# Optimization experiments

Hardware: AMD Instinct MI355X
Metric: run time of the kernel (lower is better)

Reference implementation:

```python
import jax, jax.numpy as jnp
import numpy as np

HEADS = 16
D_MODEL = 1024
D_K = D_MODEL // HEADS


def setup_inputs() -> dict:
    key = jax.random.key(0)
    ks = jax.random.split(key, 8)
    B, S = 4, 2048
    scale = 1.0 / np.sqrt(D_MODEL)
    return {
        "queries": jax.random.normal(ks[0], (B, S, D_MODEL), dtype=jnp.float32),
        "keys": jax.random.normal(ks[1], (B, S, D_MODEL), dtype=jnp.float32),
        "values": jax.random.normal(ks[2], (B, S, D_MODEL), dtype=jnp.float32),
        # Per-head projection weights, stacked over heads: [H, d_model, d_k]
        "Wq": jax.random.normal(ks[3], (HEADS, D_MODEL, D_K), dtype=jnp.float32) * scale,
        "Wk": jax.random.normal(ks[4], (HEADS, D_MODEL, D_K), dtype=jnp.float32) * scale,
        "Wv": jax.random.normal(ks[5], (HEADS, D_MODEL, D_K), dtype=jnp.float32) * scale,
        "Wout": jax.random.normal(ks[6], (D_MODEL, D_MODEL), dtype=jnp.float32) * scale,
        "bout": jax.random.normal(ks[7], (D_MODEL,), dtype=jnp.float32) * 0.01,
    }


def reference(queries, keys, values, Wq, Wk, Wv, Wout, bout):
    # Per-head linear projections (torch Linear: x @ W.T, here W stored as [H, d_model, d_k])
    q = jnp.einsum("bsd,hdk->bhsk", queries, Wq)   # [B,H,S,d_k]
    k = jnp.einsum("btd,hdk->bhtk", keys, Wk)      # [B,H,T,d_k]
    v = jnp.einsum("btd,hdv->bhtv", values, Wv)    # [B,H,T,d_v]
    scores = jnp.einsum("bhsk,bhtk->bhst", q, k) / jnp.sqrt(jnp.float32(D_K))
    probs = jax.nn.softmax(scores, axis=-1)        # [B,H,S,T]
    wv = jnp.einsum("bhst,bhtv->bhsv", probs, v)   # [B,H,S,d_v]
    # concat heads along last dim: [B,S,H*d_v] == [B,S,d_model]
    B, H, S, Dv = wv.shape
    concat = jnp.transpose(wv, (0, 2, 1, 3)).reshape(B, S, H * Dv)
    return concat @ Wout.T + bout
```

## Files before the change

### kernel.cpp

```cpp
#include <hip/hip_runtime.h>
#include <hip/hip_bf16.h>
#include <stdint.h>

#define DM 1024
#define SZ ((size_t)8192*1024)
#define WSZ ((size_t)1024*1024)

typedef float  f32x4  __attribute__((ext_vector_type(4)));
typedef float  f32x16 __attribute__((ext_vector_type(16)));
typedef __bf16 bf16x8 __attribute__((ext_vector_type(8)));
typedef __bf16 bf16x2 __attribute__((ext_vector_type(2)));
typedef short  s16x8  __attribute__((ext_vector_type(8)));
typedef unsigned int u32;
typedef unsigned int u32x4 __attribute__((ext_vector_type(4)));

typedef const __attribute__((address_space(1))) void* gas_ptr;
typedef __attribute__((address_space(3))) void* las_ptr;

static __device__ __forceinline__ f32x4 mfma16(s16x8 a, s16x8 b, f32x4 c){
  return __builtin_amdgcn_mfma_f32_16x16x32_bf16(
      __builtin_bit_cast(bf16x8, a), __builtin_bit_cast(bf16x8, b), c, 0, 0, 0);
}
static __device__ __forceinline__ f32x16 mfma32(s16x8 a, s16x8 b, f32x16 c){
  return __builtin_amdgcn_mfma_f32_32x32x16_bf16(
      __builtin_bit_cast(bf16x8, a), __builtin_bit_cast(bf16x8, b), c, 0, 0, 0);
}

static __device__ __forceinline__ u32 pack2(float a, float b){
  bf16x2 v = { (__bf16)a, (__bf16)b };
  return __builtin_bit_cast(u32, v);
}
static __device__ __forceinline__ short f2bf(float f){
  __bf16 v = (__bf16)f;
  return __builtin_bit_cast(short, v);
}

static __device__ __forceinline__ void gload_lds16(void* l, const void* g){
  __builtin_amdgcn_global_load_lds((gas_ptr)g, (las_ptr)l, 16, 0, 0);
}

#define QSCALE 0.1803368801111444f


__global__ void convert_misc(const float* __restrict__ q, const float* __restrict__ k,
                             const float* __restrict__ v, const float* __restrict__ wo,
                             short* __restrict__ ws){
  size_t c = (size_t)blockIdx.x*blockDim.x + threadIdx.x;
  const size_t n8_in = 3*(SZ/8);
  const float* src; short* dst;
  if (c < n8_in){
    int s = (int)(c >> 20);
    size_t off = c*8 - ((size_t)s << 23);
    src = (s==0 ? q : (s==1 ? k : v)) + off;
    dst = ws + c*8;
  } else {
    size_t off = (c - n8_in)*8;
    src = wo + off;
    dst = ws + 6*SZ + 3*WSZ + off;
  }
  float4 a = *(const float4*)src;
  float4 b = *(const float4*)(src + 4);
  uint4 o;
  o.x = pack2(a.x, a.y); o.y = pack2(a.z, a.w);
  o.z = pack2(b.x, b.y); o.w = pack2(b.z, b.w);
  *(uint4*)dst = o;
}

__global__ void convert_wqkv(const float* __restrict__ wq, const float* __restrict__ wk,
                             const float* __restrict__ wv, short* __restrict__ ws){
  __shared__ float tile[64][65];
  int bid = blockIdx.x;
  int sel = bid >> 8;
  int h   = (bid >> 4) & 15;
  int dt  = bid & 15;
  const float* W = sel==0 ? wq : (sel==1 ? wk : wv);
  float sc = sel==0 ? QSCALE : 1.0f;
  short* Bt = ws + 6*SZ + (size_t)sel*WSZ;
  int tid = threadIdx.x;
  int r = tid >> 4, c4 = (tid & 15)*4;
  int d0 = dt*64;
  #pragma unroll
  for (int i=0;i<4;i++){
    int d = r + i*16;
    float4 vv = *(const float4*)&W[(size_t)h*65536 + (size_t)(d0+d)*64 + c4];
    tile[d][c4+0]=vv.x*sc; tile[d][c4+1]=vv.y*sc; tile[d][c4+2]=vv.z*sc; tile[d][c4+3]=vv.w*sc;
  }
  __syncthreads();
  #pragma unroll
  for (int i=0;i<4;i++){
    int kk = r + i*16;
    unsigned int lo = pack2(tile[c4+0][kk], tile[c4+1][kk]);
    unsigned int hi = pack2(tile[c4+2][kk], tile[c4+3][kk]);
    *(uint2*)&Bt[(size_t)(h*64+kk)*1024 + d0 + c4] = make_uint2(lo, hi);
  }
}


static __device__ __forceinline__ void gemm_core_bf16(
    const short* __restrict__ A, const short* __restrict__ Bt,
    int bm, int bn, short* As, short* Bs, f32x4 acc[4][4])
{
  int tid = threadIdx.x;
  int w = tid>>6, lane = tid&63;
  int wm = w>>1, wn = w&1;
  int col = lane&15, kg = lane>>4;
  int rs = w*16 + (lane>>2);
  int ch = lane&3;
  int chs = ch ^ (rs & 3);

  auto stage = [&](int buf, int kt){
    #pragma unroll
    for (int it=0; it<2; ++it){
      int r = rs + it*64;
      gload_lds16(As + buf*4096 + r*32 + ch*8,
                  A + (size_t)(bm*128 + r)*1024 + kt*32 + chs*8);
    }
    #pragma unroll
    for (int it=0; it<2; ++it){
      int r = rs + it*64;
      gload_lds16(Bs + buf*4096 + r*32 + ch*8,
                  Bt + (size_t)(bn*128 + r)*1024 + kt*32 + chs*8);
    }
  };

  const f32x4 fzero = {0.f,0.f,0.f,0.f};
  #pragma unroll
  for (int mf=0; mf<4; ++mf)
    #pragma unroll
    for (int nf=0; nf<4; ++nf)
      acc[mf][nf] = fzero;

  int fbase = col*32 + ((kg ^ (col&3))<<3);

  stage(0, 0);
  int buf = 0;
  for (int kt=0; kt<32; ++kt){
    __syncthreads();
    if (kt < 31) stage(buf^1, kt+1);
    s16x8 af[4], bfr[4];
    #pragma unroll
    for (int mf=0; mf<4; ++mf)
      af[mf] = *(const s16x8*)(As + buf*4096 + (wm*64 + mf*16)*32 + fbase);
    #pragma unroll
    for (int nf=0; nf<4; ++nf)
      bfr[nf] = *(const s16x8*)(Bs + buf*4096 + (wn*64 + nf*16)*32 + fbase);
    #pragma unroll
    for (int mf=0; mf<4; ++mf)
      #pragma unroll
      for (int nf=0; nf<4; ++nf)
        acc[mf][nf] = mfma16(af[mf], bfr[nf], acc[mf][nf]);
    buf ^= 1;
  }
}

__global__ __launch_bounds__(256,2) void gemm_qkv(short* __restrict__ ws){
  __shared__ __align__(16) short As[2*4096];
  __shared__ __align__(16) short Bs[2*4096];
  int bid = blockIdx.x;
  bid = (bid & 7)*192 + (bid >> 3);
  int bm = bid / 24, bnq = bid % 24;
  int sel = bnq >> 3, bn = bnq & 7;
  const short* A  = ws + (size_t)sel*SZ;
  const short* Bt = ws + 6*SZ + (size_t)sel*WSZ;
  f32x4 acc[4][4];
  gemm_core_bf16(A, Bt, bm, bn, As, Bs, acc);

  int tid = threadIdx.x, w = tid>>6, lane = tid&63;
  int wm=w>>1, wn=w&1, col=lane&15, kg=lane>>4;
  if (sel == 0){
    short* O = ws + 3*SZ;
    #pragma unroll
    for (int mf=0; mf<4; ++mf){
      int gr0 = bm*128 + wm*64 + mf*16 + kg*4;
      #pragma unroll
      for (int nf=0; nf<4; ++nf){
        int gc = bn*128 + wn*64 + nf*16 + col;
        #pragma unroll
        for (int r=0; r<4; ++r)
          O[(size_t)(gr0+r)*1024 + gc] = f2bf(acc[mf][nf][r]);
      }
    }
  } else if (sel == 1){
    short* Kt = ws + 4*SZ;
    #pragma unroll
    for (int mf=0; mf<4; ++mf){
      int gr0 = bm*128 + wm*64 + mf*16 + kg*4;
      int b = gr0 >> 11, s0 = gr0 & 2047;
      int ts = s0 >> 5, t0 = s0 & 31;
      #pragma unroll
      for (int nf=0; nf<4; ++nf){
        int gc = bn*128 + wn*64 + nf*16 + col;
        int h = gc >> 6, d = gc & 63;
        size_t base = ((size_t)((b*16+h)*64 + ts))*2048 + (size_t)((d>>3)*32)*8 + (d&7);
        #pragma unroll
        for (int r=0; r<4; ++r)
          Kt[base + (size_t)(t0+r)*8] = f2bf(acc[mf][nf][r]);
      }
    }
  } else {
    short* Vt = ws + 5*SZ;
    #pragma unroll
    for (int mf=0; mf<4; ++mf){
      int gr0 = bm*128 + wm*64 + mf*16 + kg*4;
      int b = gr0 >> 11, s0 = gr0 & 2047;
      int ts = s0 >> 5, c2 = (s0 >> 3) & 3, j0 = s0 & 7;
      #pragma unroll
      for (int nf=0; nf<4; ++nf){
        int gc = bn*128 + wn*64 + nf*16 + col;
        int h = gc >> 6, dv = gc & 63;
        unsigned int lo = pack2(acc[mf][nf][0], acc[mf][nf][1]);
        unsigned int hi = pack2(acc[mf][nf][2], acc[mf][nf][3]);
        size_t addr = ((size_t)((b*16+h)*64 + ts))*2048 + (size_t)(c2*64 + dv)*8 + j0;
        *(uint2*)&Vt[addr] = make_uint2(lo, hi);
      }
    }
  }
}

__global__ __launch_bounds__(256,2) void gemm_out(const short* __restrict__ cc,
                                                  const short* __restrict__ BtO,
                                                  const float* __restrict__ bias,
                                                  float* __restrict__ out){
  __shared__ __align__(16) short As[2*4096];
  __shared__ __align__(16) short Bs[2*4096];
  int bid = blockIdx.x;
  bid = (bid & 7)*64 + (bid >> 3);
  int bm = bid >> 3, bn = bid & 7;
  f32x4 acc[4][4];
  gemm_core_bf16(cc, BtO, bm, bn, As, Bs, acc);

  int tid = threadIdx.x, w=tid>>6, lane=tid&63;
  int wm=w>>1, wn=w&1, col=lane&15, kg=lane>>4;
  #pragma unroll
  for (int nf=0; nf<4; ++nf){
    int gc = bn*128 + wn*64 + nf*16 + col;
    float bb = bias[gc];
    #pragma unroll
    for (int mf=0; mf<4; ++mf){
      int gr0 = bm*128 + wm*64 + mf*16 + kg*4;
      #pragma unroll
      for (int r=0; r<4; ++r)
        out[(size_t)(gr0+r)*1024 + gc] = acc[mf][nf][r] + bb;
    }
  }
}

__global__ __launch_bounds__(256,2) void attn(const short* __restrict__ qp,
                                              const short* __restrict__ kpT,
                                              const short* __restrict__ vTt,
                                              short* __restrict__ cc){
  __shared__ __align__(16) short Ks[2][2048];
  __shared__ __align__(16) short Vs[2][2048];
  int bid = blockIdx.x;
  bid = (bid & 7)*64 + (bid >> 3);
  int qb = bid & 7, h = (bid>>3) & 15, b = bid >> 7;
  int bh = b*16 + h;
  int tid = threadIdx.x, w = tid>>6, lane = tid&63;
  int ql = lane & 31, hi = lane >> 5;
  int qbase = qb*256 + w*64;

  const short* qg = qp + ((size_t)(b*2048 + qbase + ql))*1024 + h*64;
  s16x8 qf[2][4];
  #pragma unroll
  for (int qt=0; qt<2; ++qt)
    #pragma unroll
    for (int ks=0; ks<4; ++ks)
      qf[qt][ks] = *(const s16x8*)(qg + qt*32*1024 + ks*16 + hi*8);

  const short* ktb = kpT + ((size_t)(bh*64))*2048;
  const short* vtb = vTt + ((size_t)(bh*64))*2048;

  int koff = hi*512 + ql*16;
  int voff = hi*1024 + ql*16;

  int jj = (w & 1) * 1024;
  const short* ksrcb = ktb + jj + lane*8;
  const short* vsrcb = vtb + jj + lane*8;
  auto stageK = [&](int buf, int ti){
    if (w < 2){
      const short* src = ksrcb + (size_t)ti*2048;
      short* dst = &Ks[buf][jj + lane*8];
      gload_lds16(dst, src);
      gload_lds16(dst + 512, src + 512);
    }
  };
  auto stageV = [&](int buf, int ti){
    if (w >= 2){
      const short* src = vsrcb + (size_t)ti*2048;
      short* dst = &Vs[buf][jj + lane*8];
      gload_lds16(dst, src);
      gload_lds16(dst + 512, src + 512);
    }
  };

  const f32x16 z16 = {0.f,0.f,0.f,0.f,0.f,0.f,0.f,0.f,
                      0.f,0.f,0.f,0.f,0.f,0.f,0.f,0.f};
  f32x16 o[2][2] = {{z16, z16}, {z16, z16}};
  float l0 = 0.f, l1 = 0.f;
  f32x16 sA0, sA1, sB0, sB1;

  auto packP = [&](f32x16& s, s16x8* pb){
    u32 a0 = pack2(s[0], s[1]),  b0 = pack2(s[2], s[3]);
    u32 c0 = pack2(s[4], s[5]),  d0 = pack2(s[6], s[7]);
    asm("v_permlane32_swap_b32 %0, %1" : "+v"(a0), "+v"(c0));
    asm("v_permlane32_swap_b32 %0, %1" : "+v"(b0), "+v"(d0));
    u32x4 t0v = {a0, b0, c0, d0};
    pb[0] = __builtin_bit_cast(s16x8, t0v);
    u32 a1 = pack2(s[8], s[9]),   b1 = pack2(s[10], s[11]);
    u32 c1 = pack2(s[12], s[13]), d1 = pack2(s[14], s[15]);
    asm("v_permlane32_swap_b32 %0, %1" : "+v"(a1), "+v"(c1));
    asm("v_permlane32_swap_b32 %0, %1" : "+v"(b1), "+v"(d1));
    u32x4 t1v = {a1, b1, c1, d1};
    pb[1] = __builtin_bit_cast(s16x8, t1v);
  };

  auto iter = [&](int t, int bufV, int bufKn,
                  f32x16& si0, f32x16& si1, f32x16& so0, f32x16& so1){
    __syncthreads();
    if (t+2 < 64) stageK(bufV, t+2);
    if (t+1 < 64) stageV(bufKn, t+1);

    float la=0.f, lb=0.f, lc=0.f, ld=0.f;
    #pragma unroll
    for (int i=0;i<16;i+=4){
      si0[i]   = __builtin_amdgcn_exp2f(si0[i]);   la += si0[i];
      si0[i+1] = __builtin_amdgcn_exp2f(si0[i+1]); lb += si0[i+1];
      si0[i+2] = __builtin_amdgcn_exp2f(si0[i+2]); lc += si0[i+2];
      si0[i+3] = __builtin_amdgcn_exp2f(si0[i+3]); ld += si0[i+3];
    }
    l0 += (la+lb)+(lc+ld);
    float le=0.f, lf=0.f, lg=0.f, lh=0.f;
    #pragma unroll
    for (int i=0;i<16;i+=4){
      si1[i]   = __builtin_amdgcn_exp2f(si1[i]);   le += si1[i];
      si1[i+1] = __builtin_amdgcn_exp2f(si1[i+1]); lf += si1[i+1];
      si1[i+2] = __builtin_amdgcn_exp2f(si1[i+2]); lg += si1[i+2];
      si1[i+3] = __builtin_amdgcn_exp2f(si1[i+3]); lh += si1[i+3];
    }
    l1 += (le+lf)+(lg+lh);

    s16x8 pb0[2], pb1[2];
    packP(si0, pb0);
    packP(si1, pb1);

    const char* kt = (const char*)(&Ks[bufKn][0]);
    const char* vt = (const char*)(&Vs[bufV][0]);
    __builtin_amdgcn_s_setprio(1);
    so0 = z16; so1 = z16;
    if (t+1 < 64){
      #pragma unroll
      for (int ks=0; ks<4; ++ks){
        s16x8 kf = *(const s16x8*)(kt + koff + ks*1024);
        so0 = mfma32(kf, qf[0][ks], so0);
        so1 = mfma32(kf, qf[1][ks], so1);
      }
    }
    #pragma unroll
    for (int ks2=0; ks2<2; ++ks2){
      #pragma unroll
      for (int dvt=0; dvt<2; ++dvt){
        s16x8 vf = *(const s16x8*)(vt + voff + ks2*2048 + dvt*512);
        o[0][dvt] = mfma32(vf, pb0[ks2], o[0][dvt]);
        o[1][dvt] = mfma32(vf, pb1[ks2], o[1][dvt]);
      }
    }
    __builtin_amdgcn_s_setprio(0);
  };

  stageK(0, 0);
  stageV(0, 0);
  stageK(1, 1);
  __syncthreads();
  {
    const char* kt = (const char*)(&Ks[0][0]);
    sA0 = z16; sA1 = z16;
    #pragma unroll
    for (int ks=0; ks<4; ++ks){
      s16x8 kf = *(const s16x8*)(kt + koff + ks*1024);
      sA0 = mfma32(kf, qf[0][ks], sA0);
      sA1 = mfma32(kf, qf[1][ks], sA1);
    }
  }
  for (int t = 0; t < 64; t += 2){
    iter(t,   0, 1, sA0, sA1, sB0, sB1);
    iter(t+1, 1, 0, sB0, sB1, sA0, sA1);
  }

  l0 += __shfl_xor(l0, 32);
  l1 += __shfl_xor(l1, 32);
  float rc0 = 1.0f / l0, rc1 = 1.0f / l1;
  #pragma unroll
  for (int qt=0; qt<2; ++qt){
    float rcl = qt ? rc1 : rc0;
    short* og = cc + ((size_t)(b*2048 + qbase + qt*32 + ql))*1024 + h*64;
    #pragma unroll
    for (int dvt=0; dvt<2; ++dvt){
      #pragma unroll
      for (int s=0; s<4; ++s){
        int dv0 = dvt*32 + s*8 + hi*4;
        uint2 wd;
        wd.x = pack2(o[qt][dvt][s*4+0]*rcl, o[qt][dvt][s*4+1]*rcl);
        wd.y = pack2(o[qt][dvt][s*4+2]*rcl, o[qt][dvt][s*4+3]*rcl);
        *(uint2*)&og[dv0] = wd;
      }
    }
  }
}


extern "C" void kernel_launch(void* const* d_in, const int* in_sizes, int n_in,
                              void* d_out, int out_size, void* d_ws, size_t ws_size,
                              hipStream_t stream){
  const float* q  = (const float*)d_in[0];
  const float* k  = (const float*)d_in[1];
  const float* v  = (const float*)d_in[2];
  const float* wq = (const float*)d_in[3];
  const float* wk = (const float*)d_in[4];
  const float* wv = (const float*)d_in[5];
  const float* wo = (const float*)d_in[6];
  const float* bo = (const float*)d_in[7];
  short* ws = (short*)d_ws;
  float* out = (float*)d_out;

  size_t needed = (6*SZ + 4*WSZ)*sizeof(short);
  if (ws_size < needed) return;

  convert_misc<<<12800, 256, 0, stream>>>(q, k, v, wo, ws);
  convert_wqkv<<<768, 256, 0, stream>>>(wq, wk, wv, ws);
  gemm_qkv<<<1536, 256, 0, stream>>>(ws);
  attn<<<512, 256, 0, stream>>>(ws + 3*SZ, ws + 4*SZ, ws + 5*SZ, ws);
  gemm_out<<<512, 256, 0, stream>>>(ws, ws + 6*SZ + 3*WSZ, bo, out);
}
```

Baseline: 199.7 us.

## Halve per-wave query tile in attention to double blocks and occupancy

The attention kernel now gives each wave 32 query rows instead of 64, so a block covers 128 queries and the grid doubles to 1024 blocks. Launch bounds rise from 2 to 4 blocks per CU, and the per-thread score, output and Q-fragment registers are halved. The aim is more blocks in flight and better latency hiding on the GPU. The cost is that every K/V tile loaded into LDS feeds half as many MFMAs, so total K/V traffic and barrier count per unit of work double.

```diff
diff --git a/kernel.cpp b/kernel.cpp
--- a/kernel.cpp
+++ b/kernel.cpp
@@ -245,27 +245,25 @@
   }
 }
 
-__global__ __launch_bounds__(256,2) void attn(const short* __restrict__ qp,
+__global__ __launch_bounds__(256,4) void attn(const short* __restrict__ qp,
                                               const short* __restrict__ kpT,
                                               const short* __restrict__ vTt,
                                               short* __restrict__ cc){
   __shared__ __align__(16) short Ks[2][2048];
   __shared__ __align__(16) short Vs[2][2048];
   int bid = blockIdx.x;
-  bid = (bid & 7)*64 + (bid >> 3);
-  int qb = bid & 7, h = (bid>>3) & 15, b = bid >> 7;
+  bid = (bid & 7)*128 + (bid >> 3);
+  int qb = bid & 15, h = (bid>>4) & 15, b = bid >> 8;
   int bh = b*16 + h;
   int tid = threadIdx.x, w = tid>>6, lane = tid&63;
   int ql = lane & 31, hi = lane >> 5;
-  int qbase = qb*256 + w*64;
+  int qbase = qb*128 + w*32;
 
   const short* qg = qp + ((size_t)(b*2048 + qbase + ql))*1024 + h*64;
-  s16x8 qf[2][4];
-  #pragma unroll
-  for (int qt=0; qt<2; ++qt)
-    #pragma unroll
-    for (int ks=0; ks<4; ++ks)
-      qf[qt][ks] = *(const s16x8*)(qg + qt*32*1024 + ks*16 + hi*8);
+  s16x8 qf[4];
+  #pragma unroll
+  for (int ks=0; ks<4; ++ks)
+    qf[ks] = *(const s16x8*)(qg + ks*16 + hi*8);
 
   const short* ktb = kpT + ((size_t)(bh*64))*2048;
   const short* vtb = vTt + ((size_t)(bh*64))*2048;
@@ -295,9 +293,9 @@
 
   const f32x16 z16 = {0.f,0.f,0.f,0.f,0.f,0.f,0.f,0.f,
                       0.f,0.f,0.f,0.f,0.f,0.f,0.f,0.f};
-  f32x16 o[2][2] = {{z16, z16}, {z16, z16}};
-  float l0 = 0.f, l1 = 0.f;
-  f32x16 sA0, sA1, sB0, sB1;
+  f32x16 o0 = z16, o1 = z16;
+  float l = 0.f;
+  f32x16 sA, sB;
 
   auto packP = [&](f32x16& s, s16x8* pb){
     u32 a0 = pack2(s[0], s[1]),  b0 = pack2(s[2], s[3]);
@@ -314,8 +312,7 @@
     pb[1] = __builtin_bit_cast(s16x8, t1v);
   };
 
-  auto iter = [&](int t, int bufV, int bufKn,
-                  f32x16& si0, f32x16& si1, f32x16& so0, f32x16& so1){
+  auto iter = [&](int t, int bufV, int bufKn, f32x16& si, f32x16& so){
     __syncthreads();
     if (t+2 < 64) stageK(bufV, t+2);
     if (t+1 < 64) stageV(bufKn, t+1);
@@ -323,46 +320,33 @@
     float la=0.f, lb=0.f, lc=0.f, ld=0.f;
     #pragma unroll
     for (int i=0;i<16;i+=4){
-      si0[i]   = __builtin_amdgcn_exp2f(si0[i]);   la += si0[i];
-      si0[i+1] = __builtin_amdgcn_exp2f(si0[i+1]); lb += si0[i+1];
-      si0[i+2] = __builtin_amdgcn_exp2f(si0[i+2]); lc += si0[i+2];
-      si0[i+3] = __builtin_amdgcn_exp2f(si0[i+3]); ld += si0[i+3];
-    }
-    l0 += (la+lb)+(lc+ld);
-    float le=0.f, lf=0.f, lg=0.f, lh=0.f;
-    #pragma unroll
-    for (int i=0;i<16;i+=4){
-      si1[i]   = __builtin_amdgcn_exp2f(si1[i]);   le += si1[i];
-      si1[i+1] = __builtin_amdgcn_exp2f(si1[i+1]); lf += si1[i+1];
-      si1[i+2] = __builtin_amdgcn_exp2f(si1[i+2]); lg += si1[i+2];
-      si1[i+3] = __builtin_amdgcn_exp2f(si1[i+3]); lh += si1[i+3];
-    }
-    l1 += (le+lf)+(lg+lh);
-
-    s16x8 pb0[2], pb1[2];
-    packP(si0, pb0);
-    packP(si1, pb1);
+      si[i]   = __builtin_amdgcn_exp2f(si[i]);   la += si[i];
+      si[i+1] = __builtin_amdgcn_exp2f(si[i+1]); lb += si[i+1];
+      si[i+2] = __builtin_amdgcn_exp2f(si[i+2]); lc += si[i+2];
+      si[i+3] = __builtin_amdgcn_exp2f(si[i+3]); ld += si[i+3];
+    }
+    l += (la+lb)+(lc+ld);
+
+    s16x8 pb[2];
+    packP(si, pb);
 
     const char* kt = (const char*)(&Ks[bufKn][0]);
     const char* vt = (const char*)(&Vs[bufV][0]);
     __builtin_amdgcn_s_setprio(1);
-    so0 = z16; so1 = z16;
+    so = z16;
     if (t+1 < 64){
       #pragma unroll
       for (int ks=0; ks<4; ++ks){
         s16x8 kf = *(const s16x8*)(kt + koff + ks*1024);
-        so0 = mfma32(kf, qf[0][ks], so0);
-        so1 = mfma32(kf, qf[1][ks], so1);
+        so = mfma32(kf, qf[ks], so);
       }
     }
     #pragma unroll
     for (int ks2=0; ks2<2; ++ks2){
-      #pragma unroll
-      for (int dvt=0; dvt<2; ++dvt){
-        s16x8 vf = *(const s16x8*)(vt + voff + ks2*2048 + dvt*512);
-        o[0][dvt] = mfma32(vf, pb0[ks2], o[0][dvt]);
-        o[1][dvt] = mfma32(vf, pb1[ks2], o[1][dvt]);
-      }
+      s16x8 vf0 = *(const s16x8*)(vt + voff + ks2*2048);
+      s16x8 vf1 = *(const s16x8*)(vt + voff + ks2*2048 + 512);
+      o0 = mfma32(vf0, pb[ks2], o0);
+      o1 = mfma32(vf1, pb[ks2], o1);
     }
     __builtin_amdgcn_s_setprio(0);
   };
@@ -373,37 +357,31 @@
   __syncthreads();
   {
     const char* kt = (const char*)(&Ks[0][0]);
-    sA0 = z16; sA1 = z16;
+    sA = z16;
     #pragma unroll
     for (int ks=0; ks<4; ++ks){
       s16x8 kf = *(const s16x8*)(kt + koff + ks*1024);
-      sA0 = mfma32(kf, qf[0][ks], sA0);
-      sA1 = mfma32(kf, qf[1][ks], sA1);
+      sA = mfma32(kf, qf[ks], sA);
     }
   }
   for (int t = 0; t < 64; t += 2){
-    iter(t,   0, 1, sA0, sA1, sB0, sB1);
-    iter(t+1, 1, 0, sB0, sB1, sA0, sA1);
-  }
-
-  l0 += __shfl_xor(l0, 32);
-  l1 += __shfl_xor(l1, 32);
-  float rc0 = 1.0f / l0, rc1 = 1.0f / l1;
-  #pragma unroll
-  for (int qt=0; qt<2; ++qt){
-    float rcl = qt ? rc1 : rc0;
-    short* og = cc + ((size_t)(b*2048 + qbase + qt*32 + ql))*1024 + h*64;
-    #pragma unroll
-    for (int dvt=0; dvt<2; ++dvt){
-      #pragma unroll
-      for (int s=0; s<4; ++s){
-        int dv0 = dvt*32 + s*8 + hi*4;
-        uint2 wd;
-        wd.x = pack2(o[qt][dvt][s*4+0]*rcl, o[qt][dvt][s*4+1]*rcl);
-        wd.y = pack2(o[qt][dvt][s*4+2]*rcl, o[qt][dvt][s*4+3]*rcl);
-        *(uint2*)&og[dv0] = wd;
-      }
-    }
+    iter(t,   0, 1, sA, sB);
+    iter(t+1, 1, 0, sB, sA);
+  }
+
+  l += __shfl_xor(l, 32);
+  float rcl = 1.0f / l;
+  short* og = cc + ((size_t)(b*2048 + qbase + ql))*1024 + h*64;
+  #pragma unroll
+  for (int s=0; s<4; ++s){
+    int dv0 = s*8 + hi*4;
+    uint2 w0, w1;
+    w0.x = pack2(o0[s*4+0]*rcl, o0[s*4+1]*rcl);
+    w0.y = pack2(o0[s*4+2]*rcl, o0[s*4+3]*rcl);
+    *(uint2*)&og[dv0] = w0;
+    w1.x = pack2(o1[s*4+0]*rcl, o1[s*4+1]*rcl);
+    w1.y = pack2(o1[s*4+2]*rcl, o1[s*4+3]*rcl);
+    *(uint2*)&og[32 + dv0] = w1;
   }
 }
 
@@ -428,6 +406,6 @@
   convert_misc<<<12800, 256, 0, stream>>>(q, k, v, wo, ws);
   convert_wqkv<<<768, 256, 0, stream>>>(wq, wk, wv, ws);
   gemm_qkv<<<1536, 256, 0, stream>>>(ws);
-  attn<<<512, 256, 0, stream>>>(ws + 3*SZ, ws + 4*SZ, ws + 5*SZ, ws);
+  attn<<<1024, 256, 0, stream>>>(ws + 3*SZ, ws + 4*SZ, ws + 5*SZ, ws);
   gemm_out<<<512, 256, 0, stream>>>(ws, ws + 6*SZ + 3*WSZ, bo, out);
 }
```

After: 204.8 us. 1.03x slower.
